# Performance work log

Measured on AMD Instinct MI355X. Metric: run time of the kernel, lower is better.

Reference implementation:

```python
import jax, jax.numpy as jnp
import numpy as np

B, N, D = 8, 1024, 768
H, Z = 12, 64          # num_heads, head_dim (D = H*Z)
HID = 3072             # int(D * mlp_ratio)


def setup_inputs() -> dict:
    key = jax.random.key(0)
    k1, k2, k3, k4 = jax.random.split(key, 4)
    s = 0.02
    x = jax.random.normal(k1, (B, N, D), dtype=jnp.float32)
    Wq = jax.random.normal(k2, (D, D), dtype=jnp.float32) * s
    Wk = jax.random.normal(k3, (D, D), dtype=jnp.float32) * s
    betas = jnp.full((H,), Z ** -0.5, dtype=jnp.float32)
    W_mlp = jax.random.normal(k4, (HID, D), dtype=jnp.float32) * s
    return {"x": x, "Wq": Wq, "Wk": Wk, "betas": betas, "W_mlp": W_mlp}


def reference(x, Wq, Wk, betas, W_mlp):
    # --- KQ-aligned attention ---
    # torch Linear: y = x @ W.T ; weight shape [out=D, in=D]
    Q = jnp.einsum('bnd,ed->bne', x, Wq).reshape(B, N, H, Z).transpose(0, 2, 1, 3)  # bhqz
    K = jnp.einsum('bnd,ed->bne', x, Wk).reshape(B, N, H, Z).transpose(0, 2, 1, 3)  # bhkz
    Wq_r = Wq.reshape(H, Z, D)
    Wk_r = Wk.reshape(H, Z, D)
    F1 = jnp.einsum('hzd,bhkz->bkhd', Wq_r, K)
    F2 = jnp.einsum('hzd,bhqz->bqhd', Wk_r, Q)
    scores = jnp.einsum('bhqz,bhkz,h->bhqk', Q, K, betas)
    attn = jax.nn.softmax(scores, axis=-1)
    T1 = jnp.einsum('bkhd,bhqk->bqd', F1, attn)
    T2 = jnp.einsum('bqhd,bhqk->bkd', F2, attn)
    # --- symmetric-weight Hopfield MLP (bias=False) ---
    hid = jax.nn.relu(jnp.einsum('bnd,hd->bnh', x, W_mlp))
    mlp = jnp.einsum('bnh,hd->bnd', hid, W_mlp)
    return T1 + T2 + mlp
```

## Files before the change

kernel.cpp:

```cpp
#include <hip/hip_runtime.h>
#include <hip/hip_bf16.h>

#define Bq 8
#define Nq 1024
#define Dq 768
#define Hq 12
#define Zq 64
#define HIDq 3072
#define BN (Bq*Nq)
#define QKP 1536

typedef unsigned short u16;
typedef short s16x8 __attribute__((ext_vector_type(8)));
typedef float f32x4 __attribute__((ext_vector_type(4)));
typedef unsigned short u16x4 __attribute__((ext_vector_type(4)));

#define MFMA16 __builtin_amdgcn_mfma_f32_16x16x32_bf16
#define GLOAD16(g, l) __builtin_amdgcn_global_load_lds( \
    (const __attribute__((address_space(1))) void*)(const void*)(g), \
    (__attribute__((address_space(3))) void*)(l), 16, 0, 0)

__device__ __forceinline__ u16 f2bf(float f) {
  unsigned u = __float_as_uint(f);
  return (u16)((u + 0x7FFFu + ((u >> 16) & 1u)) >> 16);
}

__device__ __forceinline__ void xcd_swizzle(int gx, int gy, int& bx, int& by) {
  int l = blockIdx.y * gx + blockIdx.x;
  int c = l & 7, j = l >> 3;
  by = c * (gy >> 3) + j / gx;
  bx = j % gx;
}

__global__ __launch_bounds__(256) void cvt_bf16(const float* __restrict__ in,
                                                u16* __restrict__ out, int n) {
  int i = (blockIdx.x * 256 + threadIdx.x) * 4;
  if (i >= n) return;
  float4 v = *(const float4*)&in[i];
  u16x4 o; o[0] = f2bf(v.x); o[1] = f2bf(v.y); o[2] = f2bf(v.z); o[3] = f2bf(v.w);
  *(u16x4*)&out[i] = o;
}

__global__ __launch_bounds__(256) void cvt_tr(const float* __restrict__ in,
                                              u16* __restrict__ out, u16* __restrict__ outT,
                                              int C, int out_p, int outT_p) {
  __shared__ u16 T[64][72];
  const int t = threadIdx.x;
  const int r0 = blockIdx.y * 64, c0 = blockIdx.x * 64;
  const int r = t >> 3, c8 = (t & 7) * 8;
#pragma unroll
  for (int p = 0; p < 2; p++) {
    const float* ip = &in[(size_t)(r0 + r + p * 32) * C + c0 + c8];
    float4 v0 = *(const float4*)ip, v1 = *(const float4*)(ip + 4);
    u16 tmp[8] = {f2bf(v0.x), f2bf(v0.y), f2bf(v0.z), f2bf(v0.w),
                  f2bf(v1.x), f2bf(v1.y), f2bf(v1.z), f2bf(v1.w)};
    *(uint4*)&out[(size_t)(r0 + r + p * 32) * out_p + c0 + c8] = *(uint4*)tmp;
    *(uint4*)&T[r + p * 32][c8] = *(uint4*)tmp;
  }
  __syncthreads();
#pragma unroll
  for (int p = 0; p < 2; p++) {
    int oc = r + p * 32;
    u16 tmp[8];
#pragma unroll
    for (int j = 0; j < 8; j++) tmp[j] = T[c8 + j][oc];
    *(uint4*)&outT[(size_t)(c0 + oc) * outT_p + r0 + c8] = *(uint4*)tmp;
  }
}

__global__ __launch_bounds__(256) void transpose_bf16(
    const u16* __restrict__ in, u16* __restrict__ out,
    int in_pitch, int out_pitch, int inner_n,
    long in_bs_o, long in_bs_i, long out_bs_o, long out_bs_i) {
  __shared__ u16 T[64][72];
  const int t = threadIdx.x;
  const int bz = blockIdx.z;
  const long iboff = (long)(bz / inner_n) * in_bs_o + (long)(bz % inner_n) * in_bs_i;
  const long oboff = (long)(bz / inner_n) * out_bs_o + (long)(bz % inner_n) * out_bs_i;
  const u16* ip = in + iboff + (long)(blockIdx.y * 64) * in_pitch + blockIdx.x * 64;
  u16* op = out + oboff + (long)(blockIdx.x * 64) * out_pitch + blockIdx.y * 64;
  const int r = t >> 3, c8 = (t & 7) * 8;
#pragma unroll
  for (int p = 0; p < 2; p++)
    *(uint4*)&T[r + p * 32][c8] = *(const uint4*)(ip + (size_t)(r + p * 32) * in_pitch + c8);
  __syncthreads();
#pragma unroll
  for (int p = 0; p < 2; p++) {
    int oc = r + p * 32;
    u16 tmp[8];
#pragma unroll
    for (int j = 0; j < 8; j++) tmp[j] = T[c8 + j][oc];
    *(uint4*)(op + (size_t)oc * out_pitch + c8) = *(uint4*)tmp;
  }
}

template<bool RELU>
__global__ __launch_bounds__(256) void gemm_bf16(
    const u16* __restrict__ A, const u16* __restrict__ B, u16* __restrict__ C,
    int M, int N, int K) {
  __shared__ u16 As[2][128 * 32];
  __shared__ u16 Bs[2][128 * 32];
  int bx, by;
  xcd_swizzle(gridDim.x, gridDim.y, bx, by);
  const int t = threadIdx.x, l = t & 63, w = t >> 6;
  const int lq = l & 15, quad = l >> 4;
  const int bm = by * 128, bn = bx * 128;
  const int wm = (w & 1) * 64, wn = (w >> 1) * 64;
  f32x4 acc[4][4];
#pragma unroll
  for (int i = 0; i < 4; i++)
#pragma unroll
    for (int j = 0; j < 4; j++) acc[i][j] = (f32x4){0.f, 0.f, 0.f, 0.f};

  auto stage = [&](int k0, int bufi) {
#pragma unroll
    for (int p = 0; p < 2; p++) {
      int idx = p * 256 + t;
      GLOAD16(A + (size_t)(bm + (idx >> 2)) * K + k0 + (idx & 3) * 8, &As[bufi][idx * 8]);
      GLOAD16(B + (size_t)(bn + (idx >> 2)) * K + k0 + (idx & 3) * 8, &Bs[bufi][idx * 8]);
    }
  };
  stage(0, 0);
  const int nIter = K >> 5;
  for (int it = 0; it < nIter; it++) {
    __syncthreads();
    if (it + 1 < nIter) stage((it + 1) * 32, (it + 1) & 1);
    const int bi = it & 1;
    s16x8 af[4], bf[4];
#pragma unroll
    for (int mt = 0; mt < 4; mt++)
      af[mt] = *(const s16x8*)&As[bi][(wm + mt * 16 + lq) * 32 + quad * 8];
#pragma unroll
    for (int nt = 0; nt < 4; nt++)
      bf[nt] = *(const s16x8*)&Bs[bi][(wn + nt * 16 + lq) * 32 + quad * 8];
#pragma unroll
    for (int mt = 0; mt < 4; mt++)
#pragma unroll
      for (int nt = 0; nt < 4; nt++)
        acc[mt][nt] = MFMA16(af[mt], bf[nt], acc[mt][nt], 0, 0, 0);
  }
#pragma unroll
  for (int mt = 0; mt < 4; mt++)
#pragma unroll
    for (int nt = 0; nt < 4; nt++) {
      int row = bm + wm + mt * 16 + quad * 4;
      int col = bn + wn + nt * 16 + lq;
#pragma unroll
      for (int r = 0; r < 4; r++) {
        float v = acc[mt][nt][r];
        if (RELU) v = fmaxf(v, 0.f);
        C[(size_t)(row + r) * N + col] = f2bf(v);
      }
    }
}

__global__ __launch_bounds__(256) void gemm_out2(
    const u16* __restrict__ AV12, const u16* __restrict__ hid,
    const u16* __restrict__ WqkT, const u16* __restrict__ WmT,
    float* __restrict__ out) {
  __shared__ u16 As[2][128 * 64];
  __shared__ u16 Bs[2][64 * 64];
  int bx, by;
  xcd_swizzle(gridDim.x, gridDim.y, bx, by);
  const int t = threadIdx.x, l = t & 63, w = t >> 6;
  const int lq = l & 15, quad = l >> 4;
  const int bm = by * 128, bn = bx * 64;
  const int wm = w * 32;
  f32x4 acc[2][4];
#pragma unroll
  for (int i = 0; i < 2; i++)
#pragma unroll
    for (int j = 0; j < 4; j++) acc[i][j] = (f32x4){0.f, 0.f, 0.f, 0.f};

  auto stage = [&](int tl, int bufi) {
    const u16* A; const u16* B; int pitch, k0;
    if (tl < 24) { A = AV12; B = WqkT; pitch = QKP;  k0 = tl * 64; }
    else         { A = hid;  B = WmT;  pitch = HIDq; k0 = (tl - 24) * 64; }
#pragma unroll
    for (int p = 0; p < 4; p++) {
      int idx = p * 256 + t, ks = idx >> 9, rem = idx & 511;
      GLOAD16(A + (size_t)(bm + (rem >> 2)) * pitch + k0 + ks * 32 + (rem & 3) * 8,
              &As[bufi][idx * 8]);
    }
#pragma unroll
    for (int p = 0; p < 2; p++) {
      int idx = p * 256 + t, ks = idx >> 8, rem = idx & 255;
      GLOAD16(B + (size_t)(bn + (rem >> 2)) * pitch + k0 + ks * 32 + (rem & 3) * 8,
              &Bs[bufi][idx * 8]);
    }
  };
  stage(0, 0);
  for (int tl = 0; tl < 72; tl++) {
    __syncthreads();
    if (tl + 1 < 72) stage(tl + 1, (tl + 1) & 1);
    const int bi = tl & 1;
#pragma unroll
    for (int ks = 0; ks < 2; ks++) {
      s16x8 af[2], bf[4];
#pragma unroll
      for (int mt = 0; mt < 2; mt++)
        af[mt] = *(const s16x8*)&As[bi][ks * 4096 + (wm + mt * 16 + lq) * 32 + quad * 8];
#pragma unroll
      for (int nt = 0; nt < 4; nt++)
        bf[nt] = *(const s16x8*)&Bs[bi][ks * 2048 + (nt * 16 + lq) * 32 + quad * 8];
#pragma unroll
      for (int mt = 0; mt < 2; mt++)
#pragma unroll
        for (int nt = 0; nt < 4; nt++)
          acc[mt][nt] = MFMA16(af[mt], bf[nt], acc[mt][nt], 0, 0, 0);
    }
  }
#pragma unroll
  for (int mt = 0; mt < 2; mt++)
#pragma unroll
    for (int nt = 0; nt < 4; nt++) {
      int row = bm + wm + mt * 16 + quad * 4;
      int col = bn + nt * 16 + lq;
#pragma unroll
      for (int r = 0; r < 4; r++)
        out[(size_t)(row + r) * Dq + col] = acc[mt][nt][r];
    }
}

__global__ __launch_bounds__(256) void attn_pass1(
    const u16* __restrict__ QKb, const u16* __restrict__ KbT,
    const float* __restrict__ betas, u16* __restrict__ AV12,
    float* __restrict__ lg) {
  __shared__ u16 Qs[2][64][32];
  __shared__ u16 Ks[2][64][32];
  __shared__ u16 Kts[2][64][32];
  __shared__ u16 Ps[64][72];
  __shared__ float red[4][64];
  __shared__ float li[64];

  const int t = threadIdx.x, l = t & 63, w = t >> 6;
  const int lq = l & 15, quad = l >> 4;
  const int c = blockIdx.x & 7, j = blockIdx.x >> 3;
  const int bh = c * 12 + j / 16, qt = j % 16;
  const int b = bh / Hq, h = bh % Hq;
  const int q0 = qt * 64;
  const float beta = betas[h];
  const u16* Qh = QKb + (size_t)(b * Nq) * QKP + h * 64;
  const u16* Kh = Qh + Dq;
  const u16* KTh = KbT + (size_t)bh * 64 * Nq;
  u16* QsF = &Qs[0][0][0]; u16* KsF = &Ks[0][0][0]; u16* KtsF = &Kts[0][0][0];

#pragma unroll
  for (int p = 0; p < 2; p++) {
    int idx = p * 256 + t;
    GLOAD16(Qh + (size_t)(q0 + ((idx >> 2) & 63)) * QKP + (idx >> 8) * 32 + (idx & 3) * 8,
            QsF + idx * 8);
  }
  __syncthreads();
  s16x8 bqf[2][4];
#pragma unroll
  for (int zs = 0; zs < 2; zs++)
#pragma unroll
    for (int nt = 0; nt < 4; nt++)
      bqf[zs][nt] = *(const s16x8*)&Qs[zs][nt * 16 + lq][quad * 8];

  float lsum[4] = {0.f, 0.f, 0.f, 0.f};
  f32x4 ao[4];
#pragma unroll
  for (int nt = 0; nt < 4; nt++) ao[nt] = (f32x4){0.f, 0.f, 0.f, 0.f};

  for (int kt = 0; kt < 16; kt++) {
#pragma unroll
    for (int p = 0; p < 2; p++) {
      int idx = p * 256 + t;
      GLOAD16(Kh + (size_t)(kt * 64 + ((idx >> 2) & 63)) * QKP + (idx >> 8) * 32 + (idx & 3) * 8,
              KsF + idx * 8);
      GLOAD16(KTh + (size_t)((idx >> 2) & 63) * Nq + kt * 64 + (idx >> 8) * 32 + (idx & 3) * 8,
              KtsF + idx * 8);
    }
    __syncthreads();
    f32x4 sc[4];
#pragma unroll
    for (int nt = 0; nt < 4; nt++) sc[nt] = (f32x4){0.f, 0.f, 0.f, 0.f};
#pragma unroll
    for (int zs = 0; zs < 2; zs++) {
      s16x8 a = *(const s16x8*)&Ks[zs][w * 16 + lq][quad * 8];
#pragma unroll
      for (int nt = 0; nt < 4; nt++)
        sc[nt] = MFMA16(a, bqf[zs][nt], sc[nt], 0, 0, 0);
    }
#pragma unroll
    for (int nt = 0; nt < 4; nt++) {
      u16x4 pk;
#pragma unroll
      for (int r = 0; r < 4; r++) {
        float e = __expf(sc[nt][r] * beta);
        lsum[nt] += e;
        pk[r] = f2bf(e);
      }
      *(u16x4*)&Ps[nt * 16 + lq][w * 16 + quad * 4] = pk;
    }
    __syncthreads();
#pragma unroll
    for (int ks = 0; ks < 2; ks++) {
      s16x8 a = *(const s16x8*)&Ps[w * 16 + lq][ks * 32 + quad * 8];
#pragma unroll
      for (int nt = 0; nt < 4; nt++) {
        s16x8 bk = *(const s16x8*)&Kts[ks][nt * 16 + lq][quad * 8];
        ao[nt] = MFMA16(a, bk, ao[nt], 0, 0, 0);
      }
    }
    __syncthreads();
  }
#pragma unroll
  for (int nt = 0; nt < 4; nt++) {
    float v = lsum[nt];
    v += __shfl_xor(v, 16, 64);
    v += __shfl_xor(v, 32, 64);
    if (l < 16) red[w][nt * 16 + lq] = v;
  }
  __syncthreads();
  if (t < 64) {
    float s = red[0][t] + red[1][t] + red[2][t] + red[3][t];
    lg[(size_t)bh * Nq + q0 + t] = s;
    li[t] = 1.0f / s;
  }
  __syncthreads();
  u16* Oh = AV12 + (size_t)(b * Nq + q0) * QKP + h * 64;
  float lr[4];
#pragma unroll
  for (int r = 0; r < 4; r++) lr[r] = li[w * 16 + quad * 4 + r];
#pragma unroll
  for (int nt = 0; nt < 4; nt++)
#pragma unroll
    for (int r = 0; r < 4; r++)
      Oh[(size_t)(w * 16 + quad * 4 + r) * QKP + nt * 16 + lq] = f2bf(ao[nt][r] * lr[r]);
}

__global__ __launch_bounds__(256) void attn_pass2(
    const u16* __restrict__ QKb, const u16* __restrict__ QbT,
    const float* __restrict__ betas, u16* __restrict__ AV12,
    const float* __restrict__ lg) {
  __shared__ u16 Qs[2][64][32];
  __shared__ u16 Qts[2][64][32];
  __shared__ u16 Ks[2][64][32];
  __shared__ u16 Pts[64][72];
  __shared__ float li_s[64];

  const int t = threadIdx.x, l = t & 63, w = t >> 6;
  const int lq = l & 15, quad = l >> 4;
  const int c = blockIdx.x & 7, j = blockIdx.x >> 3;
  const int bh = c * 12 + j / 16, kt = j % 16;
  const int b = bh / Hq, h = bh % Hq;
  const int k0 = kt * 64;
  const float beta = betas[h];
  const u16* Qh = QKb + (size_t)(b * Nq) * QKP + h * 64;
  const u16* Kh = Qh + Dq;
  const u16* QTh = QbT + (size_t)bh * 64 * Nq;
  u16* QsF = &Qs[0][0][0]; u16* QtsF = &Qts[0][0][0]; u16* KsF = &Ks[0][0][0];

#pragma unroll
  for (int p = 0; p < 2; p++) {
    int idx = p * 256 + t;
    GLOAD16(Kh + (size_t)(k0 + ((idx >> 2) & 63)) * QKP + (idx >> 8) * 32 + (idx & 3) * 8,
            KsF + idx * 8);
  }
  __syncthreads();
  s16x8 bkf[2][4];
#pragma unroll
  for (int zs = 0; zs < 2; zs++)
#pragma unroll
    for (int nt = 0; nt < 4; nt++)
      bkf[zs][nt] = *(const s16x8*)&Ks[zs][nt * 16 + lq][quad * 8];

  f32x4 ao[4];
#pragma unroll
  for (int nt = 0; nt < 4; nt++) ao[nt] = (f32x4){0.f, 0.f, 0.f, 0.f};

  for (int qt = 0; qt < 16; qt++) {
#pragma unroll
    for (int p = 0; p < 2; p++) {
      int idx = p * 256 + t;
      GLOAD16(Qh + (size_t)(qt * 64 + ((idx >> 2) & 63)) * QKP + (idx >> 8) * 32 + (idx & 3) * 8,
              QsF + idx * 8);
      GLOAD16(QTh + (size_t)((idx >> 2) & 63) * Nq + qt * 64 + (idx >> 8) * 32 + (idx & 3) * 8,
              QtsF + idx * 8);
    }
    if (t < 64) li_s[t] = 1.0f / lg[(size_t)bh * Nq + qt * 64 + t];
    __syncthreads();
    f32x4 sc[4];
#pragma unroll
    for (int nt = 0; nt < 4; nt++) sc[nt] = (f32x4){0.f, 0.f, 0.f, 0.f};
#pragma unroll
    for (int zs = 0; zs < 2; zs++) {
      s16x8 a = *(const s16x8*)&Qs[zs][w * 16 + lq][quad * 8];
#pragma unroll
      for (int nt = 0; nt < 4; nt++)
        sc[nt] = MFMA16(a, bkf[zs][nt], sc[nt], 0, 0, 0);
    }
    float lr[4];
#pragma unroll
    for (int r = 0; r < 4; r++) lr[r] = li_s[w * 16 + quad * 4 + r];
#pragma unroll
    for (int nt = 0; nt < 4; nt++) {
      u16x4 pk;
#pragma unroll
      for (int r = 0; r < 4; r++)
        pk[r] = f2bf(__expf(sc[nt][r] * beta) * lr[r]);
      *(u16x4*)&Pts[nt * 16 + lq][w * 16 + quad * 4] = pk;
    }
    __syncthreads();
#pragma unroll
    for (int qs = 0; qs < 2; qs++) {
      s16x8 a = *(const s16x8*)&Pts[w * 16 + lq][qs * 32 + quad * 8];
#pragma unroll
      for (int nt = 0; nt < 4; nt++) {
        s16x8 bq = *(const s16x8*)&Qts[qs][nt * 16 + lq][quad * 8];
        ao[nt] = MFMA16(a, bq, ao[nt], 0, 0, 0);
      }
    }
    __syncthreads();
  }
  u16* Oh = AV12 + (size_t)(b * Nq + k0) * QKP + Dq + h * 64;
#pragma unroll
  for (int nt = 0; nt < 4; nt++)
#pragma unroll
    for (int r = 0; r < 4; r++)
      Oh[(size_t)(w * 16 + quad * 4 + r) * QKP + nt * 16 + lq] = f2bf(ao[nt][r]);
}

extern "C" void kernel_launch(void* const* d_in, const int* in_sizes, int n_in,
                              void* d_out, int out_size, void* d_ws, size_t ws_size,
                              hipStream_t stream) {
  const float* x     = (const float*)d_in[0];
  const float* Wq    = (const float*)d_in[1];
  const float* Wk    = (const float*)d_in[2];
  const float* betas = (const float*)d_in[3];
  const float* Wm    = (const float*)d_in[4];
  float* out = (float*)d_out;

  u16* xb   = (u16*)d_ws;
  u16* Wqkb = xb + (size_t)BN * Dq;
  u16* Wmb  = Wqkb + (size_t)QKP * Dq;
  u16* WqkT = Wmb + (size_t)HIDq * Dq;
  u16* QKb  = WqkT + (size_t)Dq * QKP;
  u16* QbT  = QKb + (size_t)BN * QKP;
  u16* KbT  = QbT + (size_t)Bq * Hq * Zq * Nq;
  u16* AV12 = KbT + (size_t)Bq * Hq * Zq * Nq;
  float* lg = (float*)(AV12 + (size_t)BN * QKP);
  u16* hidb = QKb;
  u16* WmT  = xb;

  dim3 blk(256);
  cvt_bf16<<<(BN * Dq) / 1024, blk, 0, stream>>>(x, xb, BN * Dq);
  cvt_tr<<<dim3(12, 12), blk, 0, stream>>>(Wq, Wqkb, WqkT, Dq, Dq, QKP);
  cvt_tr<<<dim3(12, 12), blk, 0, stream>>>(Wk, Wqkb + (size_t)Dq * Dq, WqkT + Dq, Dq, Dq, QKP);
  cvt_bf16<<<(HIDq * Dq) / 1024, blk, 0, stream>>>(Wm, Wmb, HIDq * Dq);

  gemm_bf16<false><<<dim3(QKP / 128, BN / 128), blk, 0, stream>>>(
      xb, Wqkb, QKb, BN, QKP, Dq);

  transpose_bf16<<<dim3(1, 16, 96), blk, 0, stream>>>(QKb, QbT, QKP, Nq, Hq,
      (long)Nq * QKP, 64, (long)Hq * 64 * Nq, (long)64 * Nq);
  transpose_bf16<<<dim3(1, 16, 96), blk, 0, stream>>>(QKb + Dq, KbT, QKP, Nq, Hq,
      (long)Nq * QKP, 64, (long)Hq * 64 * Nq, (long)64 * Nq);

  attn_pass1<<<Bq * Hq * 16, blk, 0, stream>>>(QKb, KbT, betas, AV12, lg);
  attn_pass2<<<Bq * Hq * 16, blk, 0, stream>>>(QKb, QbT, betas, AV12, lg);

  gemm_bf16<true><<<dim3(HIDq / 128, BN / 128), blk, 0, stream>>>(
      xb, Wmb, hidb, BN, HIDq, Dq);

  transpose_bf16<<<dim3(12, 48, 1), blk, 0, stream>>>(Wmb, WmT, Dq, HIDq, 1, 0, 0, 0, 0);

  gemm_out2<<<dim3(Dq / 64, BN / 128), blk, 0, stream>>>(AV12, hidb, WqkT, WmT, out);
}
```

Baseline: 364.8 us.

## Double-buffer K/Q tiles in attention passes and use 2-wave output GEMM blocks

Measured after the change: 383.4 us. +5.1%, slower.

```diff
diff --git a/kernel.cpp b/kernel.cpp
--- a/kernel.cpp
+++ b/kernel.cpp
@@ -154,21 +154,21 @@
     }
 }
 
-__global__ __launch_bounds__(256) void gemm_out2(
+__global__ __launch_bounds__(128) void gemm_out2(
     const u16* __restrict__ AV12, const u16* __restrict__ hid,
     const u16* __restrict__ WqkT, const u16* __restrict__ WmT,
     float* __restrict__ out) {
-  __shared__ u16 As[2][128 * 64];
-  __shared__ u16 Bs[2][64 * 64];
+  __shared__ u16 As[2][2 * 128 * 32];
+  __shared__ u16 Bs[2][2 * 64 * 32];
   int bx, by;
   xcd_swizzle(gridDim.x, gridDim.y, bx, by);
   const int t = threadIdx.x, l = t & 63, w = t >> 6;
   const int lq = l & 15, quad = l >> 4;
   const int bm = by * 128, bn = bx * 64;
-  const int wm = w * 32;
-  f32x4 acc[2][4];
-#pragma unroll
-  for (int i = 0; i < 2; i++)
+  const int wm = w * 64;
+  f32x4 acc[4][4];
+#pragma unroll
+  for (int i = 0; i < 4; i++)
 #pragma unroll
     for (int j = 0; j < 4; j++) acc[i][j] = (f32x4){0.f, 0.f, 0.f, 0.f};
 
@@ -177,14 +177,14 @@
     if (tl < 24) { A = AV12; B = WqkT; pitch = QKP;  k0 = tl * 64; }
     else         { A = hid;  B = WmT;  pitch = HIDq; k0 = (tl - 24) * 64; }
 #pragma unroll
-    for (int p = 0; p < 4; p++) {
-      int idx = p * 256 + t, ks = idx >> 9, rem = idx & 511;
+    for (int p = 0; p < 8; p++) {
+      int idx = p * 128 + t, ks = idx >> 9, rem = idx & 511;
       GLOAD16(A + (size_t)(bm + (rem >> 2)) * pitch + k0 + ks * 32 + (rem & 3) * 8,
               &As[bufi][idx * 8]);
     }
 #pragma unroll
-    for (int p = 0; p < 2; p++) {
-      int idx = p * 256 + t, ks = idx >> 8, rem = idx & 255;
+    for (int p = 0; p < 4; p++) {
+      int idx = p * 128 + t, ks = idx >> 8, rem = idx & 255;
       GLOAD16(B + (size_t)(bn + (rem >> 2)) * pitch + k0 + ks * 32 + (rem & 3) * 8,
               &Bs[bufi][idx * 8]);
     }
@@ -196,22 +196,22 @@
     const int bi = tl & 1;
 #pragma unroll
     for (int ks = 0; ks < 2; ks++) {
-      s16x8 af[2], bf[4];
-#pragma unroll
-      for (int mt = 0; mt < 2; mt++)
+      s16x8 af[4], bf[4];
+#pragma unroll
+      for (int mt = 0; mt < 4; mt++)
         af[mt] = *(const s16x8*)&As[bi][ks * 4096 + (wm + mt * 16 + lq) * 32 + quad * 8];
 #pragma unroll
       for (int nt = 0; nt < 4; nt++)
         bf[nt] = *(const s16x8*)&Bs[bi][ks * 2048 + (nt * 16 + lq) * 32 + quad * 8];
 #pragma unroll
-      for (int mt = 0; mt < 2; mt++)
+      for (int mt = 0; mt < 4; mt++)
 #pragma unroll
         for (int nt = 0; nt < 4; nt++)
           acc[mt][nt] = MFMA16(af[mt], bf[nt], acc[mt][nt], 0, 0, 0);
     }
   }
 #pragma unroll
-  for (int mt = 0; mt < 2; mt++)
+  for (int mt = 0; mt < 4; mt++)
 #pragma unroll
     for (int nt = 0; nt < 4; nt++) {
       int row = bm + wm + mt * 16 + quad * 4;
@@ -227,8 +227,8 @@
     const float* __restrict__ betas, u16* __restrict__ AV12,
     float* __restrict__ lg) {
   __shared__ u16 Qs[2][64][32];
-  __shared__ u16 Ks[2][64][32];
-  __shared__ u16 Kts[2][64][32];
+  __shared__ u16 Ks[2][2][64][32];
+  __shared__ u16 Kts[2][2][64][32];
   __shared__ u16 Ps[64][72];
   __shared__ float red[4][64];
   __shared__ float li[64];
@@ -243,7 +243,26 @@
   const u16* Qh = QKb + (size_t)(b * Nq) * QKP + h * 64;
   const u16* Kh = Qh + Dq;
   const u16* KTh = KbT + (size_t)bh * 64 * Nq;
-  u16* QsF = &Qs[0][0][0]; u16* KsF = &Ks[0][0][0]; u16* KtsF = &Kts[0][0][0];
+  u16* QsF = &Qs[0][0][0];
+  u16* KsF = &Ks[0][0][0][0];
+  u16* KtsF = &Kts[0][0][0][0];
+
+  auto stageK = [&](int kt, int bufi) {
+#pragma unroll
+    for (int p = 0; p < 2; p++) {
+      int idx = p * 256 + t;
+      GLOAD16(Kh + (size_t)(kt * 64 + ((idx >> 2) & 63)) * QKP + (idx >> 8) * 32 + (idx & 3) * 8,
+              KsF + bufi * 4096 + idx * 8);
+    }
+  };
+  auto stageKt = [&](int kt, int bufi) {
+#pragma unroll
+    for (int p = 0; p < 2; p++) {
+      int idx = p * 256 + t;
+      GLOAD16(KTh + (size_t)((idx >> 2) & 63) * Nq + kt * 64 + (idx >> 8) * 32 + (idx & 3) * 8,
+              KtsF + bufi * 4096 + idx * 8);
+    }
+  };
 
 #pragma unroll
   for (int p = 0; p < 2; p++) {
@@ -251,6 +270,8 @@
     GLOAD16(Qh + (size_t)(q0 + ((idx >> 2) & 63)) * QKP + (idx >> 8) * 32 + (idx & 3) * 8,
             QsF + idx * 8);
   }
+  stageK(0, 0);
+  stageKt(0, 0);
   __syncthreads();
   s16x8 bqf[2][4];
 #pragma unroll
@@ -265,21 +286,15 @@
   for (int nt = 0; nt < 4; nt++) ao[nt] = (f32x4){0.f, 0.f, 0.f, 0.f};
 
   for (int kt = 0; kt < 16; kt++) {
-#pragma unroll
-    for (int p = 0; p < 2; p++) {
-      int idx = p * 256 + t;
-      GLOAD16(Kh + (size_t)(kt * 64 + ((idx >> 2) & 63)) * QKP + (idx >> 8) * 32 + (idx & 3) * 8,
-              KsF + idx * 8);
-      GLOAD16(KTh + (size_t)((idx >> 2) & 63) * Nq + kt * 64 + (idx >> 8) * 32 + (idx & 3) * 8,
-              KtsF + idx * 8);
-    }
-    __syncthreads();
+    const int bi = kt & 1;
+    if (kt) __syncthreads();
+    if (kt + 1 < 16) stageK(kt + 1, 1 - bi);
     f32x4 sc[4];
 #pragma unroll
     for (int nt = 0; nt < 4; nt++) sc[nt] = (f32x4){0.f, 0.f, 0.f, 0.f};
 #pragma unroll
     for (int zs = 0; zs < 2; zs++) {
-      s16x8 a = *(const s16x8*)&Ks[zs][w * 16 + lq][quad * 8];
+      s16x8 a = *(const s16x8*)&Ks[bi][zs][w * 16 + lq][quad * 8];
 #pragma unroll
       for (int nt = 0; nt < 4; nt++)
         sc[nt] = MFMA16(a, bqf[zs][nt], sc[nt], 0, 0, 0);
@@ -296,17 +311,18 @@
       *(u16x4*)&Ps[nt * 16 + lq][w * 16 + quad * 4] = pk;
     }
     __syncthreads();
+    if (kt + 1 < 16) stageKt(kt + 1, 1 - bi);
 #pragma unroll
     for (int ks = 0; ks < 2; ks++) {
       s16x8 a = *(const s16x8*)&Ps[w * 16 + lq][ks * 32 + quad * 8];
 #pragma unroll
       for (int nt = 0; nt < 4; nt++) {
-        s16x8 bk = *(const s16x8*)&Kts[ks][nt * 16 + lq][quad * 8];
+        s16x8 bk = *(const s16x8*)&Kts[bi][ks][nt * 16 + lq][quad * 8];
         ao[nt] = MFMA16(a, bk, ao[nt], 0, 0, 0);
       }
     }
-    __syncthreads();
-  }
+  }
+  __syncthreads();
 #pragma unroll
   for (int nt = 0; nt < 4; nt++) {
     float v = lsum[nt];
@@ -336,11 +352,11 @@
     const u16* __restrict__ QKb, const u16* __restrict__ QbT,
     const float* __restrict__ betas, u16* __restrict__ AV12,
     const float* __restrict__ lg) {
-  __shared__ u16 Qs[2][64][32];
-  __shared__ u16 Qts[2][64][32];
+  __shared__ u16 Qs[2][2][64][32];
+  __shared__ u16 Qts[2][2][64][32];
   __shared__ u16 Ks[2][64][32];
   __shared__ u16 Pts[64][72];
-  __shared__ float li_s[64];
+  __shared__ float li_s[2][64];
 
   const int t = threadIdx.x, l = t & 63, w = t >> 6;
   const int lq = l & 15, quad = l >> 4;
@@ -352,7 +368,26 @@
   const u16* Qh = QKb + (size_t)(b * Nq) * QKP + h * 64;
   const u16* Kh = Qh + Dq;
   const u16* QTh = QbT + (size_t)bh * 64 * Nq;
-  u16* QsF = &Qs[0][0][0]; u16* QtsF = &Qts[0][0][0]; u16* KsF = &Ks[0][0][0];
+  u16* QsF = &Qs[0][0][0][0];
+  u16* QtsF = &Qts[0][0][0][0];
+  u16* KsF = &Ks[0][0][0];
+
+  auto stageQ = [&](int qt, int bufi) {
+#pragma unroll
+    for (int p = 0; p < 2; p++) {
+      int idx = p * 256 + t;
+      GLOAD16(Qh + (size_t)(qt * 64 + ((idx >> 2) & 63)) * QKP + (idx >> 8) * 32 + (idx & 3) * 8,
+              QsF + bufi * 4096 + idx * 8);
+    }
+  };
+  auto stageQt = [&](int qt, int bufi) {
+#pragma unroll
+    for (int p = 0; p < 2; p++) {
+      int idx = p * 256 + t;
+      GLOAD16(QTh + (size_t)((idx >> 2) & 63) * Nq + qt * 64 + (idx >> 8) * 32 + (idx & 3) * 8,
+              QtsF + bufi * 4096 + idx * 8);
+    }
+  };
 
 #pragma unroll
   for (int p = 0; p < 2; p++) {
@@ -360,6 +395,9 @@
     GLOAD16(Kh + (size_t)(k0 + ((idx >> 2) & 63)) * QKP + (idx >> 8) * 32 + (idx & 3) * 8,
             KsF + idx * 8);
   }
+  stageQ(0, 0);
+  stageQt(0, 0);
+  if (t < 64) li_s[0][t] = 1.0f / lg[(size_t)bh * Nq + t];
   __syncthreads();
   s16x8 bkf[2][4];
 #pragma unroll
@@ -373,29 +411,22 @@
   for (int nt = 0; nt < 4; nt++) ao[nt] = (f32x4){0.f, 0.f, 0.f, 0.f};
 
   for (int qt = 0; qt < 16; qt++) {
-#pragma unroll
-    for (int p = 0; p < 2; p++) {
-      int idx = p * 256 + t;
-      GLOAD16(Qh + (size_t)(qt * 64 + ((idx >> 2) & 63)) * QKP + (idx >> 8) * 32 + (idx & 3) * 8,
-              QsF + idx * 8);
-      GLOAD16(QTh + (size_t)((idx >> 2) & 63) * Nq + qt * 64 + (idx >> 8) * 32 + (idx & 3) * 8,
-              QtsF + idx * 8);
-    }
-    if (t < 64) li_s[t] = 1.0f / lg[(size_t)bh * Nq + qt * 64 + t];
-    __syncthreads();
+    const int bi = qt & 1;
+    if (qt) __syncthreads();
+    if (qt + 1 < 16) stageQ(qt + 1, 1 - bi);
     f32x4 sc[4];
 #pragma unroll
     for (int nt = 0; nt < 4; nt++) sc[nt] = (f32x4){0.f, 0.f, 0.f, 0.f};
 #pragma unroll
     for (int zs = 0; zs < 2; zs++) {
-      s16x8 a = *(const s16x8*)&Qs[zs][w * 16 + lq][quad * 8];
+      s16x8 a = *(const s16x8*)&Qs[bi][zs][w * 16 + lq][quad * 8];
 #pragma unroll
       for (int nt = 0; nt < 4; nt++)
         sc[nt] = MFMA16(a, bkf[zs][nt], sc[nt], 0, 0, 0);
     }
     float lr[4];
 #pragma unroll
-    for (int r = 0; r < 4; r++) lr[r] = li_s[w * 16 + quad * 4 + r];
+    for (int r = 0; r < 4; r++) lr[r] = li_s[bi][w * 16 + quad * 4 + r];
 #pragma unroll
     for (int nt = 0; nt < 4; nt++) {
       u16x4 pk;
@@ -405,16 +436,19 @@
       *(u16x4*)&Pts[nt * 16 + lq][w * 16 + quad * 4] = pk;
     }
     __syncthreads();
+    if (qt + 1 < 16) {
+      stageQt(qt + 1, 1 - bi);
+      if (t < 64) li_s[1 - bi][t] = 1.0f / lg[(size_t)bh * Nq + (qt + 1) * 64 + t];
+    }
 #pragma unroll
     for (int qs = 0; qs < 2; qs++) {
       s16x8 a = *(const s16x8*)&Pts[w * 16 + lq][qs * 32 + quad * 8];
 #pragma unroll
       for (int nt = 0; nt < 4; nt++) {
-        s16x8 bq = *(const s16x8*)&Qts[qs][nt * 16 + lq][quad * 8];
+        s16x8 bq = *(const s16x8*)&Qts[bi][qs][nt * 16 + lq][quad * 8];
         ao[nt] = MFMA16(a, bq, ao[nt], 0, 0, 0);
       }
     }
-    __syncthreads();
   }
   u16* Oh = AV12 + (size_t)(b * Nq + k0) * QKP + Dq + h * 64;
 #pragma unroll
@@ -468,5 +502,5 @@
 
   transpose_bf16<<<dim3(12, 48, 1), blk, 0, stream>>>(Wmb, WmT, Dq, HIDq, 1, 0, 0, 0, 0);
 
-  gemm_out2<<<dim3(Dq / 64, BN / 128), blk, 0, stream>>>(AV12, hidb, WqkT, WmT, out);
-}
+  gemm_out2<<<dim3(Dq / 64, BN / 128), dim3(128), 0, stream>>>(AV12, hidb, WqkT, WmT, out);
+}
```
